# Kernel tuning notes

Hardware: AMD Instinct MI355X
Metric: run time of the kernel (lower is better)

The kernel has to match this reference:

```python
import jax, jax.numpy as jnp
import numpy as np

B, S, D, H = 2, 2048, 1024, 16
DK = D // H


def setup_inputs() -> dict:
    key = jax.random.key(0)
    ks = jax.random.split(key, 6)
    scale = D ** -0.5
    return {
        "x": jax.random.normal(ks[0], (B, S, D), dtype=jnp.float32),
        "Wq": jax.random.normal(ks[1], (D, D), dtype=jnp.float32) * scale,
        "Wk": jax.random.normal(ks[2], (D, D), dtype=jnp.float32) * scale,
        "Wv": jax.random.normal(ks[3], (D, D), dtype=jnp.float32) * scale,
        "Wp": jax.random.normal(ks[4], (D, D), dtype=jnp.float32) * scale,
        "bp": jax.random.normal(ks[5], (D,), dtype=jnp.float32) * 0.01,
    }


def reference(x, Wq, Wk, Wv, Wp, bp):
    b, s, d = x.shape
    # projections (torch Linear: x @ W.T)
    q = (x @ Wq.T).reshape(b, s, H, DK).transpose(0, 2, 1, 3)  # [b,h,s,dk]
    k = (x @ Wk.T).reshape(b, s, H, DK).transpose(0, 2, 1, 3)
    v = (x @ Wv.T).reshape(b, s, H, DK).transpose(0, 2, 1, 3)
    wei = jnp.einsum('bhqd,bhkd->bhqk', q, k) * (DK ** -0.5)  # [b,h,s,s]
    causal = jnp.tril(jnp.ones((s, s), dtype=bool))
    wei = jnp.where(causal, wei, -jnp.inf)
    wei = jax.nn.softmax(wei, axis=-1)
    out = jnp.einsum('bhqk,bhkd->bhqd', wei, v)
    out = out.transpose(0, 2, 1, 3).reshape(b, s, H * DK)
    return out @ Wp.T + bp
```

## Files before the change

### kernel.cpp

```cpp
#include <hip/hip_runtime.h>
#include <hip/hip_bf16.h>

typedef short short8 __attribute__((ext_vector_type(8)));
typedef float floatx4 __attribute__((ext_vector_type(4)));
typedef float floatx16 __attribute__((ext_vector_type(16)));

#define DEV static __device__ __forceinline__

DEV unsigned short f2bf(float x) {
    union { float f; unsigned u; } v; v.f = x;
    unsigned r = v.u + 0x7FFFu + ((v.u >> 16) & 1u);
    return (unsigned short)(r >> 16);
}

DEV unsigned pk2(float lo, float hi) {
    union { __hip_bfloat162 h; unsigned u; } v;
    v.h = __float22bfloat162_rn(make_float2(lo, hi));
    return v.u;
}

DEV float fexp2(float x) {
#if __has_builtin(__builtin_amdgcn_exp2f)
    return __builtin_amdgcn_exp2f(x);
#else
    return exp2f(x);
#endif
}

DEV float bf2f(unsigned short s) {
    union { unsigned u; float f; } v; v.u = (unsigned)s << 16;
    return v.f;
}

DEV __attribute__((address_space(3))) unsigned int* lds_as3(void* p) {
    return (__attribute__((address_space(3))) unsigned int*)(unsigned int)(unsigned long long)p;
}
DEV const __attribute__((address_space(1))) unsigned int* gbl_as1(const void* p) {
    return (const __attribute__((address_space(1))) unsigned int*)(unsigned long long)p;
}

__global__ __launch_bounds__(256) void cvt_all(
    const float* __restrict__ x,  const float* __restrict__ wq,
    const float* __restrict__ wk, const float* __restrict__ wv,
    const float* __restrict__ wp,
    unsigned short* __restrict__ xb, unsigned short* __restrict__ wqkv,
    unsigned short* __restrict__ wpb)
{
    long c = (long)blockIdx.x * 256 + threadIdx.x;
    const float* src; unsigned short* dst; long off;
    if      (c <  524288) { src = x;  dst = xb;             off = c;          }
    else if (c <  655360) { src = wq; dst = wqkv;           off = c - 524288; }
    else if (c <  786432) { src = wk; dst = wqkv + 1048576; off = c - 655360; }
    else if (c <  917504) { src = wv; dst = wqkv + 2097152; off = c - 786432; }
    else                  { src = wp; dst = wpb;            off = c - 917504; }
    float4 a = ((const float4*)src)[off * 2];
    float4 b = ((const float4*)src)[off * 2 + 1];
    ushort4 r0, r1;
    r0.x = f2bf(a.x); r0.y = f2bf(a.y); r0.z = f2bf(a.z); r0.w = f2bf(a.w);
    r1.x = f2bf(b.x); r1.y = f2bf(b.y); r1.z = f2bf(b.z); r1.w = f2bf(b.w);
    ((ushort4*)dst)[off * 2]     = r0;
    ((ushort4*)dst)[off * 2 + 1] = r1;
}

template <int EPI>
__global__ __launch_bounds__(256) void gemm_bt(
    const unsigned short* __restrict__ A, const unsigned short* __restrict__ Bw,
    int M, int N, int K,
    unsigned short* __restrict__ Qd, unsigned short* __restrict__ Kd,
    unsigned short* __restrict__ Vtd,
    float* __restrict__ Cout, const float* __restrict__ bias)
{
    __shared__ unsigned short As[128 * 32];
    __shared__ unsigned short Bs[128 * 32];
    const int t    = threadIdx.x;
    const int lane = t & 63;
    const int wv   = t >> 6;
    const int wr   = (wv >> 1) * 64, wc = (wv & 1) * 64;
    const int lr   = lane & 15,      lg = lane >> 4;
    const int m0   = blockIdx.y * 128, n0 = blockIdx.x * 128;
    const int trow = t >> 2;
    const int tk   = (t & 3) * 8;

    floatx4 acc[4][4];
#pragma unroll
    for (int i = 0; i < 4; ++i)
#pragma unroll
        for (int j = 0; j < 4; ++j)
#pragma unroll
            for (int r = 0; r < 4; ++r) acc[i][j][r] = 0.f;

    for (int k0 = 0; k0 < K; k0 += 32) {
        __syncthreads();
#pragma unroll
        for (int r = 0; r < 2; ++r) {
            const unsigned short* ga = A  + (size_t)(m0 + r * 64 + trow) * K + k0 + tk;
            const unsigned short* gb = Bw + (size_t)(n0 + r * 64 + trow) * K + k0 + tk;
            __builtin_amdgcn_global_load_lds(gbl_as1(ga), lds_as3(&As[(r * 256 + t) * 8]), 16, 0, 0);
            __builtin_amdgcn_global_load_lds(gbl_as1(gb), lds_as3(&Bs[(r * 256 + t) * 8]), 16, 0, 0);
        }
        __syncthreads();
        short8 af[4], bf[4];
#pragma unroll
        for (int i = 0; i < 4; ++i) {
            af[i] = *(const short8*)&As[(wr + i * 16 + lr) * 32 + lg * 8];
            bf[i] = *(const short8*)&Bs[(wc + i * 16 + lr) * 32 + lg * 8];
        }
#pragma unroll
        for (int i = 0; i < 4; ++i)
#pragma unroll
            for (int j = 0; j < 4; ++j)
                acc[i][j] = __builtin_amdgcn_mfma_f32_16x16x32_bf16(af[i], bf[j], acc[i][j], 0, 0, 0);
    }

    if (EPI == 1) {
#pragma unroll
        for (int j = 0; j < 4; ++j) {
            int n = n0 + wc + j * 16 + lr;
            float bv = bias[n];
#pragma unroll
            for (int i = 0; i < 4; ++i) {
                int mb = m0 + wr + i * 16 + lg * 4;
#pragma unroll
                for (int r = 0; r < 4; ++r)
                    Cout[(size_t)(mb + r) * N + n] = acc[i][j][r] + bv;
            }
        }
    } else {
        const int which = n0 >> 10;
#pragma unroll
        for (int j = 0; j < 4; ++j) {
            int n = n0 + wc + j * 16 + lr;
            int h = (n & 1023) >> 6, d = n & 63;
#pragma unroll
            for (int i = 0; i < 4; ++i) {
                int mb = m0 + wr + i * 16 + lg * 4;
                int b = mb >> 11, s0 = mb & 2047;
                size_t bh = (size_t)(b * 16 + h);
                if (which == 2) {
                    ushort4 pv;
                    pv.x = f2bf(acc[i][j][0]); pv.y = f2bf(acc[i][j][1]);
                    pv.z = f2bf(acc[i][j][2]); pv.w = f2bf(acc[i][j][3]);
                    *(ushort4*)&Vtd[(bh * 64 + d) * 2048 + s0] = pv;
                } else {
                    unsigned short* dst = (which ? Kd : Qd) + (bh * 2048 + s0) * 64 + d;
#pragma unroll
                    for (int r = 0; r < 4; ++r) dst[r * 64] = f2bf(acc[i][j][r]);
                }
            }
        }
    }
}

__global__ __launch_bounds__(256) void attn_fwd(
    const unsigned short* __restrict__ Q, const unsigned short* __restrict__ Kg,
    const unsigned short* __restrict__ Vt, unsigned short* __restrict__ O,
    unsigned short* __restrict__ Opart, float* __restrict__ MLpart)
{
    __shared__ unsigned short ot[4][32][80];
    const int bh = blockIdx.x;
    const int z  = blockIdx.z;
    const int qt = (z == 0) ? blockIdx.y : (8 + blockIdx.y);
    const int t  = threadIdx.x, w = t >> 6, l = t & 63;
    const int lq = l & 31, hh = l >> 5;
    const int qw = qt * 128 + w * 32;
    const int kv0beg = (z == 2) ? 1024 : 0;
    const int kvEnd  = (z == 1) ? 992  : qw;
    const unsigned short* Qp = Q  + (size_t)bh * 2048 * 64;
    const unsigned short* Kp = Kg + (size_t)bh * 2048 * 64;
    const unsigned short* Vp = Vt + (size_t)bh * 64 * 2048;

    const float SCALE2 = 0.18033688011112042f;

    short8 qf[4];
#pragma unroll
    for (int kk = 0; kk < 4; ++kk)
        qf[kk] = *(const short8*)&Qp[(qw + lq) * 64 + kk * 16 + hh * 8];

    floatx16 o0, o1;
#pragma unroll
    for (int r = 0; r < 16; ++r) { o0[r] = 0.f; o1[r] = 0.f; }
    float mrun = -1e30f, lrun = 0.f;

    for (int kv0 = kv0beg; kv0 <= kvEnd; kv0 += 32) {
        floatx16 sa;
#pragma unroll
        for (int r = 0; r < 16; ++r) sa[r] = 0.f;
#pragma unroll
        for (int kk = 0; kk < 4; ++kk) {
            short8 kf = *(const short8*)&Kp[(kv0 + lq) * 64 + kk * 16 + hh * 8];
            sa = __builtin_amdgcn_mfma_f32_32x32x16_bf16(kf, qf[kk], sa, 0, 0, 0);
        }
        float sv[16];
        float tm = -1e30f;
        if (kv0 == qw) {
#pragma unroll
            for (int r = 0; r < 16; ++r) {
                int crow = (r & 3) + 8 * (r >> 2) + 4 * hh;
                float xx = sa[r] * SCALE2;
                if (crow > lq) xx = -1e30f;
                sv[r] = xx;
                tm = fmaxf(tm, xx);
            }
        } else {
#pragma unroll
            for (int r = 0; r < 16; ++r) {
                float xx = sa[r] * SCALE2;
                sv[r] = xx;
                tm = fmaxf(tm, xx);
            }
        }
        tm = fmaxf(tm, __shfl_xor(tm, 32));
        if (!__all(tm - mrun <= 8.f)) {
            float mn = fmaxf(mrun, tm);
            float f  = fexp2(mrun - mn);
            lrun *= f;
#pragma unroll
            for (int r = 0; r < 16; ++r) { o0[r] *= f; o1[r] *= f; }
            mrun = mn;
        }
        float ps = 0.f;
#pragma unroll
        for (int r = 0; r < 16; ++r) { sv[r] = fexp2(sv[r] - mrun); ps += sv[r]; }
        ps += __shfl_xor(ps, 32);
        lrun += ps;

#pragma unroll
        for (int c = 0; c < 2; ++c) {
            unsigned a0 = pk2(sv[c*8+0], sv[c*8+1]);
            unsigned a1 = pk2(sv[c*8+2], sv[c*8+3]);
            unsigned b0 = pk2(sv[c*8+4], sv[c*8+5]);
            unsigned b1 = pk2(sv[c*8+6], sv[c*8+7]);
            unsigned sa0 = __shfl_xor(a0, 32), sa1 = __shfl_xor(a1, 32);
            unsigned sb0 = __shfl_xor(b0, 32), sb1 = __shfl_xor(b1, 32);
            union { unsigned u[4]; short8 v; } pf;
            pf.u[0] = hh ? sb0 : a0;
            pf.u[1] = hh ? sb1 : a1;
            pf.u[2] = hh ? b0  : sa0;
            pf.u[3] = hh ? b1  : sa1;
            short8 vf0 = *(const short8*)&Vp[(size_t)(lq)      * 2048 + kv0 + c * 16 + hh * 8];
            short8 vf1 = *(const short8*)&Vp[(size_t)(32 + lq) * 2048 + kv0 + c * 16 + hh * 8];
            o0 = __builtin_amdgcn_mfma_f32_32x32x16_bf16(vf0, pf.v, o0, 0, 0, 0);
            o1 = __builtin_amdgcn_mfma_f32_32x32x16_bf16(vf1, pf.v, o1, 0, 0, 0);
        }
    }

    if (z == 0) {
        float inv = 1.f / lrun;
#pragma unroll
        for (int r = 0; r < 16; ++r) {
            int crow = (r & 3) + 8 * (r >> 2) + 4 * hh;
            ot[w][lq][crow]      = f2bf(o0[r] * inv);
            ot[w][lq][32 + crow] = f2bf(o1[r] * inv);
        }
        asm volatile("s_waitcnt lgkmcnt(0)" ::: "memory");
        const int b = bh >> 4, h = bh & 15;
        const int row = l >> 1, part = l & 1;
        size_t obase = (size_t)(b * 2048 + qw + row) * 1024 + h * 64 + part * 32;
#pragma unroll
        for (int jj = 0; jj < 4; ++jj) {
            uint4 v = *(const uint4*)&ot[w][row][part * 32 + jj * 8];
            *(uint4*)&O[obase + jj * 8] = v;
        }
    } else {
        const size_t sb = (size_t)((z - 1) * 32 + bh) * 1024;
        if (hh == 0)
            *(float2*)&MLpart[(sb + (qw - 1024) + lq) * 2] = make_float2(mrun, lrun);
#pragma unroll
        for (int r = 0; r < 16; ++r) {
            int crow = (r & 3) + 8 * (r >> 2) + 4 * hh;
            ot[w][lq][crow]      = f2bf(o0[r]);
            ot[w][lq][32 + crow] = f2bf(o1[r]);
        }
        asm volatile("s_waitcnt lgkmcnt(0)" ::: "memory");
        const int row = l >> 1, part = l & 1;
        size_t pbase = (sb + (qw - 1024) + row) * 64 + part * 32;
#pragma unroll
        for (int jj = 0; jj < 4; ++jj) {
            uint4 v = *(const uint4*)&ot[w][row][part * 32 + jj * 8];
            *(uint4*)&Opart[pbase + jj * 8] = v;
        }
    }
}

__global__ __launch_bounds__(256) void attn_merge(
    const unsigned short* __restrict__ Opart, const float* __restrict__ MLpart,
    unsigned short* __restrict__ O)
{
    const int tid = blockIdx.x * 256 + threadIdx.x;
    const int c8  = (tid & 7) * 8;
    const int q   = (tid >> 3) & 1023;
    const int bh  = tid >> 13;
    const size_t base = (size_t)bh * 1024 + q;

    float2 ml0 = *(const float2*)&MLpart[base * 2];
    float2 ml1 = *(const float2*)&MLpart[(32768 + base) * 2];
    float M  = fmaxf(ml0.x, ml1.x);
    float w0 = fexp2(ml0.x - M), w1 = fexp2(ml1.x - M);
    float inv = 1.f / (w0 * ml0.y + w1 * ml1.y);
    w0 *= inv; w1 *= inv;

    short8 a = *(const short8*)&Opart[base * 64 + c8];
    short8 b = *(const short8*)&Opart[(size_t)2097152 + base * 64 + c8];
    float o[8];
#pragma unroll
    for (int j = 0; j < 8; ++j)
        o[j] = w0 * bf2f((unsigned short)a[j]) + w1 * bf2f((unsigned short)b[j]);
    uint4 ov;
    ov.x = pk2(o[0], o[1]); ov.y = pk2(o[2], o[3]);
    ov.z = pk2(o[4], o[5]); ov.w = pk2(o[6], o[7]);
    const int bb = bh >> 4, h = bh & 15;
    *(uint4*)&O[(size_t)(bb * 2048 + 1024 + q) * 1024 + h * 64 + c8] = ov;
}

extern "C" void kernel_launch(void* const* d_in, const int* in_sizes, int n_in,
                              void* d_out, int out_size, void* d_ws, size_t ws_size,
                              hipStream_t stream)
{
    const float* x  = (const float*)d_in[0];
    const float* Wq = (const float*)d_in[1];
    const float* Wk = (const float*)d_in[2];
    const float* Wv = (const float*)d_in[3];
    const float* Wp = (const float*)d_in[4];
    const float* bp = (const float*)d_in[5];
    float* out = (float*)d_out;

    char* ws = (char*)d_ws;
    unsigned short* xb   = (unsigned short*)(ws);
    unsigned short* wqkv = (unsigned short*)(ws + 8388608);
    unsigned short* wpb  = (unsigned short*)(ws + 14680064);
    unsigned short* Qw   = (unsigned short*)(ws + 16777216);
    unsigned short* Kw   = (unsigned short*)(ws + 25165824);
    unsigned short* Vtw  = (unsigned short*)(ws + 33554432);
    unsigned short* Ow   = (unsigned short*)(ws + 41943040);
    unsigned short* Opart = xb;
    float*          MLp   = (float*)wqkv;

    cvt_all<<<4096, 256, 0, stream>>>(x, Wq, Wk, Wv, Wp, xb, wqkv, wpb);
    gemm_bt<0><<<dim3(24, 32), 256, 0, stream>>>(xb, wqkv, 4096, 3072, 1024,
                                                 Qw, Kw, Vtw, nullptr, nullptr);
    attn_fwd<<<dim3(32, 8, 3), 256, 0, stream>>>(Qw, Kw, Vtw, Ow, Opart, MLp);
    attn_merge<<<1024, 256, 0, stream>>>(Opart, MLp, Ow);
    gemm_bt<1><<<dim3(8, 32), 256, 0, stream>>>(Ow, wpb, 4096, 1024, 1024,
                                                nullptr, nullptr, nullptr, out, bp);
}
```

Before: 237.0 us.

## Prefetch next K/V tile into registers and raise MFMA wave priority

Software-pipelines the attention inner loop so the next tile's K and V fragments are loaded from global memory while the current tile's QK^T, softmax and PV run, which is meant to hide load latency behind compute. It also wraps the MFMA groups in s_setprio to favour matrix issue across waves, and turns the serial max and sum reductions into trees to shorten dependency chains. The trade is extra vector registers for double-buffered fragments, which may lower occupancy, plus one wasted load on the last iteration.

```diff
diff --git a/kernel.cpp b/kernel.cpp
--- a/kernel.cpp
+++ b/kernel.cpp
@@ -181,17 +181,38 @@
     for (int r = 0; r < 16; ++r) { o0[r] = 0.f; o1[r] = 0.f; }
     float mrun = -1e30f, lrun = 0.f;
 
+    short8 kc[4], vc[4];
+#pragma unroll
+    for (int kk = 0; kk < 4; ++kk)
+        kc[kk] = *(const short8*)&Kp[(kv0beg + lq) * 64 + kk * 16 + hh * 8];
+#pragma unroll
+    for (int c = 0; c < 2; ++c) {
+        vc[c * 2]     = *(const short8*)&Vp[(size_t)(lq)      * 2048 + kv0beg + c * 16 + hh * 8];
+        vc[c * 2 + 1] = *(const short8*)&Vp[(size_t)(32 + lq) * 2048 + kv0beg + c * 16 + hh * 8];
+    }
+
     for (int kv0 = kv0beg; kv0 <= kvEnd; kv0 += 32) {
         floatx16 sa;
 #pragma unroll
         for (int r = 0; r < 16; ++r) sa[r] = 0.f;
-#pragma unroll
-        for (int kk = 0; kk < 4; ++kk) {
-            short8 kf = *(const short8*)&Kp[(kv0 + lq) * 64 + kk * 16 + hh * 8];
-            sa = __builtin_amdgcn_mfma_f32_32x32x16_bf16(kf, qf[kk], sa, 0, 0, 0);
-        }
+        __builtin_amdgcn_s_setprio(1);
+#pragma unroll
+        for (int kk = 0; kk < 4; ++kk)
+            sa = __builtin_amdgcn_mfma_f32_32x32x16_bf16(kc[kk], qf[kk], sa, 0, 0, 0);
+        __builtin_amdgcn_s_setprio(0);
+
+        const int kvp = (kv0 + 32 <= kvEnd) ? (kv0 + 32) : kv0beg;
+        short8 kn[4], vn[4];
+#pragma unroll
+        for (int kk = 0; kk < 4; ++kk)
+            kn[kk] = *(const short8*)&Kp[(kvp + lq) * 64 + kk * 16 + hh * 8];
+#pragma unroll
+        for (int c = 0; c < 2; ++c) {
+            vn[c * 2]     = *(const short8*)&Vp[(size_t)(lq)      * 2048 + kvp + c * 16 + hh * 8];
+            vn[c * 2 + 1] = *(const short8*)&Vp[(size_t)(32 + lq) * 2048 + kvp + c * 16 + hh * 8];
+        }
+
         float sv[16];
-        float tm = -1e30f;
         if (kv0 == qw) {
 #pragma unroll
             for (int r = 0; r < 16; ++r) {
@@ -199,16 +220,17 @@
                 float xx = sa[r] * SCALE2;
                 if (crow > lq) xx = -1e30f;
                 sv[r] = xx;
-                tm = fmaxf(tm, xx);
             }
         } else {
 #pragma unroll
-            for (int r = 0; r < 16; ++r) {
-                float xx = sa[r] * SCALE2;
-                sv[r] = xx;
-                tm = fmaxf(tm, xx);
-            }
-        }
+            for (int r = 0; r < 16; ++r) sv[r] = sa[r] * SCALE2;
+        }
+        float t8[8], t4[4];
+#pragma unroll
+        for (int i = 0; i < 8; ++i) t8[i] = fmaxf(sv[i], sv[i + 8]);
+#pragma unroll
+        for (int i = 0; i < 4; ++i) t4[i] = fmaxf(t8[i], t8[i + 4]);
+        float tm = fmaxf(fmaxf(t4[0], t4[1]), fmaxf(t4[2], t4[3]));
         tm = fmaxf(tm, __shfl_xor(tm, 32));
         if (!__all(tm - mrun <= 8.f)) {
             float mn = fmaxf(mrun, tm);
@@ -218,9 +240,13 @@
             for (int r = 0; r < 16; ++r) { o0[r] *= f; o1[r] *= f; }
             mrun = mn;
         }
-        float ps = 0.f;
-#pragma unroll
-        for (int r = 0; r < 16; ++r) { sv[r] = fexp2(sv[r] - mrun); ps += sv[r]; }
+#pragma unroll
+        for (int r = 0; r < 16; ++r) sv[r] = fexp2(sv[r] - mrun);
+#pragma unroll
+        for (int i = 0; i < 8; ++i) t8[i] = sv[i] + sv[i + 8];
+#pragma unroll
+        for (int i = 0; i < 4; ++i) t4[i] = t8[i] + t8[i + 4];
+        float ps = (t4[0] + t4[1]) + (t4[2] + t4[3]);
         ps += __shfl_xor(ps, 32);
         lrun += ps;
 
@@ -237,11 +263,14 @@
             pf.u[1] = hh ? sb1 : a1;
             pf.u[2] = hh ? b0  : sa0;
             pf.u[3] = hh ? b1  : sa1;
-            short8 vf0 = *(const short8*)&Vp[(size_t)(lq)      * 2048 + kv0 + c * 16 + hh * 8];
-            short8 vf1 = *(const short8*)&Vp[(size_t)(32 + lq) * 2048 + kv0 + c * 16 + hh * 8];
-            o0 = __builtin_amdgcn_mfma_f32_32x32x16_bf16(vf0, pf.v, o0, 0, 0, 0);
-            o1 = __builtin_amdgcn_mfma_f32_32x32x16_bf16(vf1, pf.v, o1, 0, 0, 0);
-        }
+            __builtin_amdgcn_s_setprio(1);
+            o0 = __builtin_amdgcn_mfma_f32_32x32x16_bf16(vc[c * 2],     pf.v, o0, 0, 0, 0);
+            o1 = __builtin_amdgcn_mfma_f32_32x32x16_bf16(vc[c * 2 + 1], pf.v, o1, 0, 0, 0);
+            __builtin_amdgcn_s_setprio(0);
+        }
+
+#pragma unroll
+        for (int kk = 0; kk < 4; ++kk) { kc[kk] = kn[kk]; vc[kk] = vn[kk]; }
     }
 
     if (z == 0) {
```

New measurement: 232.7 us. No clear change (-1.8%).
